# Performance work log

Measured on AMD Instinct MI355X. Metric: run time of the kernel, lower is better.

The kernel has to match this reference:

```python
import jax, jax.numpy as jnp
import numpy as np

B, S, F, E, L, H, DMAX = 8, 1024, 768, 512, 4, 8, 4
HD = E // H
SCALE = HD ** -0.5
EPS = 1e-5


def setup_inputs() -> dict:
    key = jax.random.key(0)
    ks = jax.random.split(key, 20)
    std = 0.02
    inp = {
        "x": jax.random.normal(ks[0], (B, S, F), jnp.float32),
        "distances": jax.random.randint(ks[1], (B, S, S), 0, 8, jnp.int32),
        # lazily-created node-embedding Linear(F -> E)
        "Win": jax.random.normal(ks[2], (F, E), jnp.float32) * std,
        "b_in": jnp.zeros((E,), jnp.float32),
        # per-layer SGT params, stacked on leading layer dim L
        "Wq": jax.random.normal(ks[3], (L, E, E), jnp.float32) * std,
        "bq": jnp.zeros((L, E), jnp.float32),
        "Wk": jax.random.normal(ks[4], (L, E, E), jnp.float32) * std,
        "bk": jnp.zeros((L, E), jnp.float32),
        "Wv": jax.random.normal(ks[5], (L, E, E), jnp.float32) * std,
        "bv": jnp.zeros((L, E), jnp.float32),
        "Wo": jax.random.normal(ks[6], (L, E, E), jnp.float32) * std,
        "bo": jnp.zeros((L, E), jnp.float32),
        "dbias": jax.random.normal(ks[7], (L, DMAX + 1), jnp.float32) * 0.1,
        "ln_g": jnp.ones((L, E), jnp.float32),
        "ln_b": jnp.zeros((L, E), jnp.float32),
        # classifier: Linear(E, E//2) -> ReLU -> Linear(E//2, 2)
        "W1": jax.random.normal(ks[8], (E, E // 2), jnp.float32) * std,
        "b1": jnp.zeros((E // 2,), jnp.float32),
        "W2": jax.random.normal(ks[9], (E // 2, 2), jnp.float32) * std,
        "b2": jnp.zeros((2,), jnp.float32),
    }
    return inp


def _layer_norm(x, g, b):
    m = jnp.mean(x, axis=-1, keepdims=True)
    v = jnp.mean(jnp.square(x - m), axis=-1, keepdims=True)
    return (x - m) * jax.lax.rsqrt(v + EPS) * g + b


def reference(x, distances, Win, b_in, Wq, bq, Wk, bk, Wv, bv, Wo, bo,
              dbias, ln_g, ln_b, W1, b1, W2, b2):
    # input embedding: [B,S,F] -> [B,S,E]
    h = x @ Win + b_in
    d = jnp.clip(distances, 0, DMAX)  # [B,S,S] ints in [0, DMAX]
    for l in range(L):
        # QKV projections, split into heads: [B,H,S,HD]
        q = (h @ Wq[l] + bq[l]).reshape(B, S, H, HD).transpose(0, 2, 1, 3)
        k = (h @ Wk[l] + bk[l]).reshape(B, S, H, HD).transpose(0, 2, 1, 3)
        v = (h @ Wv[l] + bv[l]).reshape(B, S, H, HD).transpose(0, 2, 1, 3)
        # scores + learned distance bias (broadcast over heads)
        scores = jnp.einsum('bhsd,bhtd->bhst', q, k) * SCALE
        scores = scores + dbias[l][d][:, None, :, :]
        attn = jax.nn.softmax(scores, axis=-1)  # dropout = identity (eval)
        o = jnp.einsum('bhst,bhtd->bhsd', attn, v)
        o = o.transpose(0, 2, 1, 3).reshape(B, S, E) @ Wo[l] + bo[l]
        h = _layer_norm(h + o, ln_g[l], ln_b[l])
    # target node is at position 0 of each subgraph
    t = h[:, 0]  # [B,E]
    hid = jax.nn.relu(t @ W1 + b1)
    logits = hid @ W2 + b2  # [B,2]
    return logits
```

## Files before the change

### kernel.cpp

```cpp
#include <hip/hip_runtime.h>
#include <hip/hip_bf16.h>
#include <stdint.h>

#define B_   8
#define S_   1024
#define F_   768
#define E_   512
#define L_   4
#define H_   8
#define HD_  64
#define M_   (B_*S_)
#define SCALE_ 0.125f
#define EPS_ 1e-5f

typedef short bf8_t  __attribute__((ext_vector_type(8)));
typedef float f32x4  __attribute__((ext_vector_type(4)));

static __device__ __forceinline__ uint16_t bfbits(float f) {
    __hip_bfloat16 h = __float2bfloat16(f);
    union { __hip_bfloat16 h; uint16_t u; } cv{h};
    return cv.u;
}
static __device__ __forceinline__ uint32_t pack2bf(float lo, float hi) {
    return (uint32_t)bfbits(lo) | ((uint32_t)bfbits(hi) << 16);
}

template<int ROWS>
static __device__ __forceinline__ void stage_swz(const uint16_t* __restrict__ g, int ldK,
                                                 int k0, char* lds, int tid) {
    const int wave = tid >> 6, lane = tid & 63;
    constexpr int NI = ROWS / 8;
    constexpr int PW = NI / 4;
#pragma unroll
    for (int j = 0; j < PW; ++j) {
        const int I = wave * PW + j;
        const int m = I * 8 + (lane >> 3);
        const int slot = lane & 7;
        const int kc8 = slot ^ (m & 7);
        const uint16_t* gp = g + (size_t)m * ldK + k0 + kc8 * 8;
        __builtin_amdgcn_global_load_lds((const __attribute__((address_space(1))) void*)gp,
                                         (__attribute__((address_space(3))) void*)(lds + I * 1024),
                                         16, 0, 0);
    }
}

template<int OUT_MODE>
__global__ __launch_bounds__(256, 2)
void gemm_mfma(const uint16_t* __restrict__ A, const uint16_t* __restrict__ Wt,
               const float* __restrict__ bias, void* __restrict__ Cout,
               void* __restrict__ Cout2, int K)
{
    __shared__ __align__(16) char smA[128 * 128];
    __shared__ __align__(16) char smB[64 * 128];

    const int tid = threadIdx.x;
    const int lane = tid & 63;
    const int g = lane >> 4;
    const int l15 = lane & 15;
    const int wave = tid >> 6;
    const int wm = wave >> 1;
    const int wn = wave & 1;
    const int n0 = blockIdx.x * 64;
    const int m0 = blockIdx.y * 128;

    f32x4 acc[4][2];
#pragma unroll
    for (int i = 0; i < 4; ++i) {
        acc[i][0] = f32x4{0.f, 0.f, 0.f, 0.f};
        acc[i][1] = f32x4{0.f, 0.f, 0.f, 0.f};
    }

    for (int k0 = 0; k0 < K; k0 += 64) {
        stage_swz<128>(A  + (size_t)m0 * K, K, k0, smA, tid);
        stage_swz< 64>(Wt + (size_t)n0 * K, K, k0, smB, tid);
        __syncthreads();

#pragma unroll
        for (int c = 0; c < 2; ++c) {
            bf8_t bfr[2];
#pragma unroll
            for (int nb = 0; nb < 2; ++nb) {
                const int n = wn * 32 + nb * 16 + l15;
                const int slot = (c * 4 + g) ^ (n & 7);
                bfr[nb] = *(const bf8_t*)(smB + n * 128 + slot * 16);
            }
#pragma unroll
            for (int mi = 0; mi < 4; ++mi) {
                const int m = wm * 64 + mi * 16 + l15;
                const int slot = (c * 4 + g) ^ (m & 7);
                bf8_t af = *(const bf8_t*)(smA + m * 128 + slot * 16);
#pragma unroll
                for (int nb = 0; nb < 2; ++nb)
                    acc[mi][nb] = __builtin_amdgcn_mfma_f32_16x16x32_bf16(af, bfr[nb], acc[mi][nb], 0, 0, 0);
            }
        }
        __syncthreads();
    }

    const int colbase = n0 + wn * 32;
    float bia[2] = { bias[colbase + l15], bias[colbase + 16 + l15] };

#pragma unroll
    for (int mi = 0; mi < 4; ++mi) {
#pragma unroll
        for (int nb = 0; nb < 2; ++nb) {
            const int col  = colbase + nb * 16 + l15;
            const int row0 = m0 + wm * 64 + mi * 16 + g * 4;
            f32x4 v = acc[mi][nb];
            const float r0 = v.x + bia[nb], r1 = v.y + bia[nb];
            const float r2 = v.z + bia[nb], r3 = v.w + bia[nb];
            if (OUT_MODE == 1) {
                float* C = (float*)Cout;
                C[(size_t)(row0+0)*E_ + col] = r0;
                C[(size_t)(row0+1)*E_ + col] = r1;
                C[(size_t)(row0+2)*E_ + col] = r2;
                C[(size_t)(row0+3)*E_ + col] = r3;
            } else {
                float* C = (float*)Cout;
                uint16_t* C2 = (uint16_t*)Cout2;
                C[(size_t)(row0+0)*E_ + col] = r0;
                C[(size_t)(row0+1)*E_ + col] = r1;
                C[(size_t)(row0+2)*E_ + col] = r2;
                C[(size_t)(row0+3)*E_ + col] = r3;
                C2[(size_t)(row0+0)*E_ + col] = bfbits(r0);
                C2[(size_t)(row0+1)*E_ + col] = bfbits(r1);
                C2[(size_t)(row0+2)*E_ + col] = bfbits(r2);
                C2[(size_t)(row0+3)*E_ + col] = bfbits(r3);
            }
        }
    }
}

__global__ __launch_bounds__(256, 2)
void gemm_qkv(const uint16_t* __restrict__ A, const uint16_t* __restrict__ Wt,
              const float* __restrict__ bqp, const float* __restrict__ bkp,
              const float* __restrict__ bvp,
              uint16_t* __restrict__ qb, uint16_t* __restrict__ kb,
              uint16_t* __restrict__ vTb)
{
    __shared__ __align__(16) char smA[128 * 128];
    __shared__ __align__(16) char smB[64 * 128];

    const int tid = threadIdx.x;
    const int lane = tid & 63;
    const int g = lane >> 4;
    const int l15 = lane & 15;
    const int wave = tid >> 6;
    const int wm = wave >> 1;
    const int wn = wave & 1;
    const int n0 = blockIdx.x * 64;
    const int m0 = blockIdx.y * 128;
    const int sec = n0 >> 9;

    f32x4 acc[4][2];
#pragma unroll
    for (int i = 0; i < 4; ++i) {
        acc[i][0] = f32x4{0.f, 0.f, 0.f, 0.f};
        acc[i][1] = f32x4{0.f, 0.f, 0.f, 0.f};
    }

    for (int k0 = 0; k0 < E_; k0 += 64) {
        stage_swz<128>(A  + (size_t)m0 * E_, E_, k0, smA, tid);
        stage_swz< 64>(Wt + (size_t)n0 * E_, E_, k0, smB, tid);
        __syncthreads();

#pragma unroll
        for (int c = 0; c < 2; ++c) {
            bf8_t bfr[2];
#pragma unroll
            for (int nb = 0; nb < 2; ++nb) {
                const int n = wn * 32 + nb * 16 + l15;
                const int slot = (c * 4 + g) ^ (n & 7);
                bfr[nb] = *(const bf8_t*)(smB + n * 128 + slot * 16);
            }
#pragma unroll
            for (int mi = 0; mi < 4; ++mi) {
                const int m = wm * 64 + mi * 16 + l15;
                const int slot = (c * 4 + g) ^ (m & 7);
                bf8_t af = *(const bf8_t*)(smA + m * 128 + slot * 16);
#pragma unroll
                for (int nb = 0; nb < 2; ++nb)
                    acc[mi][nb] = __builtin_amdgcn_mfma_f32_16x16x32_bf16(af, bfr[nb], acc[mi][nb], 0, 0, 0);
            }
        }
        __syncthreads();
    }

    const float* bp = sec == 0 ? bqp : sec == 1 ? bkp : bvp;
    const int colbase = n0 + wn * 32;
    const int cb511 = colbase & 511;
    float bia[2] = { bp[cb511 + l15], bp[cb511 + 16 + l15] };

#pragma unroll
    for (int mi = 0; mi < 4; ++mi) {
#pragma unroll
        for (int nb = 0; nb < 2; ++nb) {
            const int col  = cb511 + nb * 16 + l15;
            const int row0 = m0 + wm * 64 + mi * 16 + g * 4;
            f32x4 v = acc[mi][nb];
            const float r0 = v.x + bia[nb], r1 = v.y + bia[nb];
            const float r2 = v.z + bia[nb], r3 = v.w + bia[nb];
            if (sec < 2) {
                uint16_t* C = sec == 0 ? qb : kb;
                C[(size_t)(row0+0)*E_ + col] = bfbits(r0);
                C[(size_t)(row0+1)*E_ + col] = bfbits(r1);
                C[(size_t)(row0+2)*E_ + col] = bfbits(r2);
                C[(size_t)(row0+3)*E_ + col] = bfbits(r3);
            } else {
                const int b  = row0 >> 10;
                const int s0 = row0 & 1023;
                uint2 val{pack2bf(r0, r1), pack2bf(r2, r3)};
                *(uint2*)&vTb[((size_t)(b * E_ + col)) * S_ + s0] = val;
            }
        }
    }
}

__global__ __launch_bounds__(256, 3)
void attn_mfma(const uint16_t* __restrict__ q, const uint16_t* __restrict__ k,
               const uint16_t* __restrict__ vT, const uint8_t* __restrict__ dT,
               const float* __restrict__ dbias, int layer, uint16_t* __restrict__ ob)
{
    __shared__ __align__(16) char Kb[2][64 * 128];
    __shared__ __align__(16) char Vb[2][64 * 128];

    const int tid = threadIdx.x, lane = tid & 63;
    const int g = lane >> 4, l15 = lane & 15, wq = tid >> 6;
    const int bid = blockIdx.x;
    const int qt = bid & 15, hh = (bid >> 4) & 7, b = bid >> 7;
    const int qrow = qt * 64 + wq * 16 + l15;

    const float db0 = dbias[layer*5+0], db1 = dbias[layer*5+1], db2 = dbias[layer*5+2],
                db3 = dbias[layer*5+3], db4 = dbias[layer*5+4];

    bf8_t qf[2];
    const uint16_t* qbase = q + ((size_t)(b * S_ + qrow)) * E_ + hh * 64;
#pragma unroll
    for (int c = 0; c < 2; ++c) qf[c] = *(const bf8_t*)(qbase + c * 32 + g * 8);

    f32x4 accO[4];
#pragma unroll
    for (int f = 0; f < 4; ++f) accO[f] = f32x4{0.f, 0.f, 0.f, 0.f};
    float mrun = -1e30f, lrun = 0.f;

    const uint16_t* kTile = k  + ((size_t)(b * S_)) * E_ + hh * 64;
    const uint16_t* vTile = vT + ((size_t)(b * E_ + hh * 64)) * S_;
    const uint8_t*  dbase = dT + ((size_t)(b * S_)) * S_ + qt * 64 + wq * 16 + l15;

    stage_swz<64>(kTile, E_, 0, Kb[0], tid);
    stage_swz<64>(vTile, S_, 0, Vb[0], tid);
    int dcur[16];
#pragma unroll
    for (int f = 0; f < 4; ++f)
#pragma unroll
        for (int r = 0; r < 4; ++r)
            dcur[f*4+r] = dbase[(size_t)(f*16 + g*4 + r) * S_];
    __syncthreads();

    for (int t = 0; t < 16; ++t) {
        const int cur = t & 1;
        char* kc_ = Kb[cur];
        char* vc_ = Vb[cur];
        if (t < 15) {
            stage_swz<64>(kTile + (size_t)(t + 1) * 64 * E_, E_, 0, Kb[cur ^ 1], tid);
            stage_swz<64>(vTile, S_, (t + 1) * 64, Vb[cur ^ 1], tid);
        }
        int dnxt[16];
#pragma unroll
        for (int f = 0; f < 4; ++f)
#pragma unroll
            for (int r = 0; r < 4; ++r)
                dnxt[f*4+r] = (t < 15) ? (int)dbase[(size_t)((t+1)*64 + f*16 + g*4 + r) * S_] : 0;

        f32x4 sc[4];
#pragma unroll
        for (int f = 0; f < 4; ++f) sc[f] = f32x4{0.f, 0.f, 0.f, 0.f};
        __builtin_amdgcn_s_setprio(1);
#pragma unroll
        for (int f = 0; f < 4; ++f) {
#pragma unroll
            for (int c = 0; c < 2; ++c) {
                const int slot = (c * 4 + g) ^ (l15 & 7);
                bf8_t kf = *(const bf8_t*)(kc_ + (f*16 + l15) * 128 + slot * 16);
                sc[f] = __builtin_amdgcn_mfma_f32_16x16x32_bf16(kf, qf[c], sc[f], 0, 0, 0);
            }
        }
        __builtin_amdgcn_s_setprio(0);

        float p[4][4];
        float tmax = -1e30f;
#pragma unroll
        for (int f = 0; f < 4; ++f) {
#pragma unroll
            for (int r = 0; r < 4; ++r) {
                const int d = dcur[f*4+r];
                const float bsel = d==0 ? db0 : d==1 ? db1 : d==2 ? db2 : d==3 ? db3 : db4;
                const float sv = fmaf(sc[f][r], SCALE_, bsel);
                p[f][r] = sv;
                tmax = fmaxf(tmax, sv);
            }
        }
        tmax = fmaxf(tmax, __shfl_xor(tmax, 16, 64));
        tmax = fmaxf(tmax, __shfl_xor(tmax, 32, 64));
        const float mnew = fmaxf(mrun, tmax);
        const float corr = __expf(mrun - mnew);
        float psum = 0.f;
#pragma unroll
        for (int f = 0; f < 4; ++f)
#pragma unroll
            for (int r = 0; r < 4; ++r) {
                p[f][r] = __expf(p[f][r] - mnew);
                psum += p[f][r];
            }
        psum += __shfl_xor(psum, 16, 64);
        psum += __shfl_xor(psum, 32, 64);
        lrun = fmaf(lrun, corr, psum);
        mrun = mnew;
#pragma unroll
        for (int f = 0; f < 4; ++f) accO[f] *= corr;

        uint32_t pk[4][2];
#pragma unroll
        for (int f = 0; f < 4; ++f) {
            pk[f][0] = pack2bf(p[f][0], p[f][1]);
            pk[f][1] = pack2bf(p[f][2], p[f][3]);
        }
        bf8_t pB[2];
#pragma unroll
        for (int c = 0; c < 2; ++c) {
            union { uint32_t w[4]; bf8_t v; } u;
#pragma unroll
            for (int j = 0; j < 4; ++j) {
                const int src = (((2*g + (j >> 1)) & 3) * 16) + l15;
                const uint32_t a  = (uint32_t)__shfl((int)pk[c*2+0][j & 1], src, 64);
                const uint32_t bb = (uint32_t)__shfl((int)pk[c*2+1][j & 1], src, 64);
                u.w[j] = (g >= 2) ? bb : a;
            }
            pB[c] = u.v;
        }

        __builtin_amdgcn_s_setprio(1);
#pragma unroll
        for (int c = 0; c < 2; ++c) {
#pragma unroll
            for (int f = 0; f < 4; ++f) {
                const int slot = (c * 4 + g) ^ (l15 & 7);
                bf8_t vf = *(const bf8_t*)(vc_ + (f*16 + l15) * 128 + slot * 16);
                accO[f] = __builtin_amdgcn_mfma_f32_16x16x32_bf16(vf, pB[c], accO[f], 0, 0, 0);
            }
        }
        __builtin_amdgcn_s_setprio(0);

        __syncthreads();
#pragma unroll
        for (int i = 0; i < 16; ++i) dcur[i] = dnxt[i];
    }

    const float inv = 1.f / lrun;
    uint16_t* obase = ob + ((size_t)(b * S_ + qrow)) * E_ + hh * 64;
#pragma unroll
    for (int f = 0; f < 4; ++f) {
        f32x4 v = accO[f];
        uint2 val{pack2bf(v.x * inv, v.y * inv), pack2bf(v.z * inv, v.w * inv)};
        *(uint2*)(obase + f * 16 + g * 4) = val;
    }
}

__global__ __launch_bounds__(256, 4)
void dist_transpose(const int* __restrict__ dist, uint8_t* __restrict__ dT)
{
    __shared__ uint8_t sT[64][64];
    const int tid = threadIdx.x;
    const int q0 = blockIdx.x * 64, t0 = blockIdx.y * 64, b = blockIdx.z;
    const int r = tid >> 4, c4 = tid & 15;
#pragma unroll
    for (int i = 0; i < 4; ++i) {
        const int qq = r + i * 16;
        int4 d4 = *(const int4*)&dist[((size_t)(b * S_ + q0 + qq)) * S_ + t0 + c4 * 4];
        sT[c4*4+0][qq] = (uint8_t)min(max(d4.x, 0), 4);
        sT[c4*4+1][qq] = (uint8_t)min(max(d4.y, 0), 4);
        sT[c4*4+2][qq] = (uint8_t)min(max(d4.z, 0), 4);
        sT[c4*4+3][qq] = (uint8_t)min(max(d4.w, 0), 4);
    }
    __syncthreads();
    const int kk = tid >> 2, qc = tid & 3;
    int4 v = *(const int4*)&sT[kk][qc * 16];
    *(int4*)&dT[((size_t)(b * S_ + t0 + kk)) * S_ + q0 + qc * 16] = v;
}

__global__ void convert_bf16(const float* __restrict__ src, uint16_t* __restrict__ dst, int n8)
{
    const int i = blockIdx.x * 256 + threadIdx.x;
    if (i >= n8) return;
    float4 a = *(const float4*)&src[(size_t)i * 8];
    float4 b = *(const float4*)&src[(size_t)i * 8 + 4];
    uint4 o{pack2bf(a.x, a.y), pack2bf(a.z, a.w), pack2bf(b.x, b.y), pack2bf(b.z, b.w)};
    *(uint4*)&dst[(size_t)i * 8] = o;
}

__global__ __launch_bounds__(256, 2)
void wtrans(const float* __restrict__ Win, const float* __restrict__ Wq,
            const float* __restrict__ Wk, const float* __restrict__ Wv,
            const float* __restrict__ Wo, uint16_t* __restrict__ Wt)
{
    __shared__ float ls[64][65];
    const int idx = blockIdx.z;
    const int Ki = (idx == 0) ? F_ : E_;
    if (blockIdx.x * 64 >= Ki) return;
    const float* src;
    size_t dstoff;
    if (idx == 0) { src = Win; dstoff = 0; }
    else {
        const int l = (idx - 1) >> 2, which = (idx - 1) & 3;
        if (which == 0)      { src = Wq + (size_t)l*E_*E_; dstoff = (size_t)F_*E_ + (size_t)(l*3+0)*E_*E_; }
        else if (which == 1) { src = Wk + (size_t)l*E_*E_; dstoff = (size_t)F_*E_ + (size_t)(l*3+1)*E_*E_; }
        else if (which == 2) { src = Wv + (size_t)l*E_*E_; dstoff = (size_t)F_*E_ + (size_t)(l*3+2)*E_*E_; }
        else                 { src = Wo + (size_t)l*E_*E_; dstoff = (size_t)F_*E_ + (size_t)12*E_*E_ + (size_t)l*E_*E_; }
    }
    uint16_t* dst = Wt + dstoff;
    const int k0 = blockIdx.x * 64, n0 = blockIdx.y * 64;
    const int tid = threadIdx.x;
    const int r = tid >> 4, c4 = tid & 15;
#pragma unroll
    for (int i = 0; i < 4; ++i)
        *(float4*)&ls[r + i*16][c4*4] = *(const float4*)&src[(size_t)(k0 + r + i*16) * E_ + n0 + c4*4];
    __syncthreads();
#pragma unroll
    for (int i = 0; i < 2; ++i) {
        const int chunk = tid + 256 * i;
        const int n = chunk >> 3, kc = chunk & 7;
        uint4 o{pack2bf(ls[kc*8+0][n], ls[kc*8+1][n]),
                pack2bf(ls[kc*8+2][n], ls[kc*8+3][n]),
                pack2bf(ls[kc*8+4][n], ls[kc*8+5][n]),
                pack2bf(ls[kc*8+6][n], ls[kc*8+7][n])};
        *(uint4*)&dst[((size_t)(n0 + n)) * Ki + k0 + kc * 8] = o;
    }
}

__global__ __launch_bounds__(256, 8)
void residual_ln(float* __restrict__ h, const float* __restrict__ o,
                 const float* __restrict__ g, const float* __restrict__ beta,
                 uint16_t* __restrict__ hb)
{
    const int wave = threadIdx.x >> 6;
    const int lane = threadIdx.x & 63;
    const int row  = blockIdx.x * 4 + wave;

    float* hr = h + (size_t)row * E_;
    const float* orow = o + (size_t)row * E_;

    float x[8];
    {
        float4 a  = *(const float4*)&hr[lane*4];
        float4 b4 = *(const float4*)&hr[256 + lane*4];
        float4 oa = *(const float4*)&orow[lane*4];
        float4 obv = *(const float4*)&orow[256 + lane*4];
        x[0] = a.x + oa.x; x[1] = a.y + oa.y; x[2] = a.z + oa.z; x[3] = a.w + oa.w;
        x[4] = b4.x + obv.x; x[5] = b4.y + obv.y; x[6] = b4.z + obv.z; x[7] = b4.w + obv.w;
    }
    float sum = 0.f, sq = 0.f;
#pragma unroll
    for (int i = 0; i < 8; ++i) { sum += x[i]; sq += x[i]*x[i]; }
#pragma unroll
    for (int off = 1; off < 64; off <<= 1) {
        sum += __shfl_xor(sum, off, 64);
        sq  += __shfl_xor(sq,  off, 64);
    }
    const float mean = sum * (1.f/512.f);
    const float var  = sq * (1.f/512.f) - mean*mean;
    const float inv  = rsqrtf(var + EPS_);

    float4 g0 = *(const float4*)&g[lane*4];
    float4 g1 = *(const float4*)&g[256 + lane*4];
    float4 be0 = *(const float4*)&beta[lane*4];
    float4 be1 = *(const float4*)&beta[256 + lane*4];

    float4 y0, y1;
    y0.x = (x[0]-mean)*inv*g0.x + be0.x;
    y0.y = (x[1]-mean)*inv*g0.y + be0.y;
    y0.z = (x[2]-mean)*inv*g0.z + be0.z;
    y0.w = (x[3]-mean)*inv*g0.w + be0.w;
    y1.x = (x[4]-mean)*inv*g1.x + be1.x;
    y1.y = (x[5]-mean)*inv*g1.y + be1.y;
    y1.z = (x[6]-mean)*inv*g1.z + be1.z;
    y1.w = (x[7]-mean)*inv*g1.w + be1.w;
    *(float4*)&hr[lane*4] = y0;
    *(float4*)&hr[256 + lane*4] = y1;

    uint16_t* hrow = hb + (size_t)row * E_;
    uint2 p0{pack2bf(y0.x, y0.y), pack2bf(y0.z, y0.w)};
    uint2 p1{pack2bf(y1.x, y1.y), pack2bf(y1.z, y1.w)};
    *(uint2*)&hrow[lane*4]       = p0;
    *(uint2*)&hrow[256 + lane*4] = p1;
}

__global__ __launch_bounds__(256, 1)
void head_kernel(const float* __restrict__ h, const float* __restrict__ W1,
                 const float* __restrict__ b1, const float* __restrict__ W2,
                 const float* __restrict__ b2, float* __restrict__ out)
{
    __shared__ float tl[512];
    __shared__ float red[8];
    const int tid = threadIdx.x;
    const int b = blockIdx.x;

    const float* hr = h + (size_t)b * S_ * E_;
    *(float2*)&tl[tid*2] = *(const float2*)&hr[tid*2];
    __syncthreads();

    float acc = b1[tid];
    for (int kk = 0; kk < 512; ++kk)
        acc = fmaf(tl[kk], W1[kk * 256 + tid], acc);
    float hid = fmaxf(acc, 0.f);

    float p0 = hid * W2[tid*2 + 0];
    float p1 = hid * W2[tid*2 + 1];
#pragma unroll
    for (int off = 32; off; off >>= 1) {
        p0 += __shfl_down(p0, off, 64);
        p1 += __shfl_down(p1, off, 64);
    }
    if ((tid & 63) == 0) {
        red[(tid >> 6)*2 + 0] = p0;
        red[(tid >> 6)*2 + 1] = p1;
    }
    __syncthreads();
    if (tid == 0) {
        out[b*2 + 0] = red[0] + red[2] + red[4] + red[6] + b2[0];
        out[b*2 + 1] = red[1] + red[3] + red[5] + red[7] + b2[1];
    }
}

extern "C" void kernel_launch(void* const* d_in, const int* in_sizes, int n_in,
                              void* d_out, int out_size, void* d_ws, size_t ws_size,
                              hipStream_t stream)
{
    const float* x     = (const float*)d_in[0];
    const int*   dist  = (const int*)  d_in[1];
    const float* Win   = (const float*)d_in[2];
    const float* b_in  = (const float*)d_in[3];
    const float* Wq    = (const float*)d_in[4];
    const float* bq    = (const float*)d_in[5];
    const float* Wk    = (const float*)d_in[6];
    const float* bk    = (const float*)d_in[7];
    const float* Wv    = (const float*)d_in[8];
    const float* bv    = (const float*)d_in[9];
    const float* Wo    = (const float*)d_in[10];
    const float* bo    = (const float*)d_in[11];
    const float* dbias = (const float*)d_in[12];
    const float* ln_g  = (const float*)d_in[13];
    const float* ln_b  = (const float*)d_in[14];
    const float* W1    = (const float*)d_in[15];
    const float* b1    = (const float*)d_in[16];
    const float* W2    = (const float*)d_in[17];
    const float* b2    = (const float*)d_in[18];
    float* out = (float*)d_out;

    char* w8 = (char*)d_ws;
    float*    h    = (float*)   (w8);
    float*    pb   = (float*)   (w8 + (size_t)(16<<20));
    uint16_t* hbf  = (uint16_t*)(w8 + (size_t)(32<<20));
    uint16_t* qb   = (uint16_t*)(w8 + (size_t)(40<<20));
    uint16_t* kb   = (uint16_t*)(w8 + (size_t)(48<<20));
    uint16_t* vTb  = (uint16_t*)(w8 + (size_t)(56<<20));
    uint16_t* obuf = (uint16_t*)(w8 + (size_t)(64<<20));
    uint16_t* xb   = (uint16_t*)(w8 + (size_t)(72<<20));
    uint16_t* Wt   = (uint16_t*)(w8 + (size_t)(84<<20));
    uint8_t*  dT   = (uint8_t*) (w8 + (size_t)(93<<20));

    const dim3 blk(256);
    const dim3 ggrid(E_/64, M_/128);
    const dim3 qkvgrid(3*E_/64, M_/128);

    convert_bf16<<<dim3(M_*F_/8/256), blk, 0, stream>>>(x, xb, M_*F_/8);
    wtrans<<<dim3(12, 8, 17), blk, 0, stream>>>(Win, Wq, Wk, Wv, Wo, Wt);
    dist_transpose<<<dim3(16, 16, 8), blk, 0, stream>>>(dist, dT);

    gemm_mfma<2><<<ggrid, blk, 0, stream>>>(xb, Wt, b_in, h, hbf, F_);

    for (int l = 0; l < L_; ++l) {
        const uint16_t* Wqkv = Wt + (size_t)F_*E_ + (size_t)(l*3)*E_*E_;
        const uint16_t* Wto  = Wt + (size_t)F_*E_ + (size_t)12*E_*E_ + (size_t)l*E_*E_;
        gemm_qkv<<<qkvgrid, blk, 0, stream>>>(hbf, Wqkv, bq + l*E_, bk + l*E_, bv + l*E_,
                                              qb, kb, vTb);
        attn_mfma<<<dim3(B_*H_*16), blk, 0, stream>>>(qb, kb, vTb, dT, dbias, l, obuf);
        gemm_mfma<1><<<ggrid, blk, 0, stream>>>(obuf, Wto, bo + l*E_, pb, nullptr, E_);
        residual_ln<<<dim3(M_/4), blk, 0, stream>>>(h, pb, ln_g + l*E_, ln_b + l*E_, hbf);
    }

    head_kernel<<<dim3(B_), blk, 0, stream>>>(h, W1, b1, W2, b2, out);
}
```

Before: 615.7 us.

## Precompute bf16 distance bias, fold scale into Q, lazy softmax rescale, wider QKV tiles

Replaces the transposed uint8 distance map with a per-layer bf16 bias tensor, already scaled by log2e, that attention adds directly into the score accumulators. The softmax scale times log2e is folded into Q in the QKV GEMM epilogue, so attention can use exp2 and drops its per-element bias selection and multiply. The running-max rescale is skipped unless the new max exceeds the old one by a threshold. Separately, the QKV GEMM tile widens to 128 columns, the attention block order is remapped, and attention occupancy is raised. The trade-off is extra memory traffic each layer, since the int32 distances are reread and a 16 MB bias is written and then read, plus bf16 rounding of the bias values.

```diff
diff --git a/kernel.cpp b/kernel.cpp
--- a/kernel.cpp
+++ b/kernel.cpp
@@ -10,8 +10,9 @@
 #define H_   8
 #define HD_  64
 #define M_   (B_*S_)
-#define SCALE_ 0.125f
 #define EPS_ 1e-5f
+#define LOG2E_ 1.44269504089f
+#define SL2E_  (0.125f * LOG2E_)
 
 typedef short bf8_t  __attribute__((ext_vector_type(8)));
 typedef float f32x4  __attribute__((ext_vector_type(4)));
@@ -23,6 +24,10 @@
 }
 static __device__ __forceinline__ uint32_t pack2bf(float lo, float hi) {
     return (uint32_t)bfbits(lo) | ((uint32_t)bfbits(hi) << 16);
+}
+static __device__ __forceinline__ float asf(uint32_t u) {
+    union { uint32_t u; float f; } cv{u};
+    return cv.f;
 }
 
 template<int ROWS>
@@ -139,7 +144,7 @@
               uint16_t* __restrict__ vTb)
 {
     __shared__ __align__(16) char smA[128 * 128];
-    __shared__ __align__(16) char smB[64 * 128];
+    __shared__ __align__(16) char smB[128 * 128];
 
     const int tid = threadIdx.x;
     const int lane = tid & 63;
@@ -148,30 +153,28 @@
     const int wave = tid >> 6;
     const int wm = wave >> 1;
     const int wn = wave & 1;
-    const int n0 = blockIdx.x * 64;
+    const int n0 = blockIdx.x * 128;
     const int m0 = blockIdx.y * 128;
-    const int sec = n0 >> 9;
-
-    f32x4 acc[4][2];
-#pragma unroll
-    for (int i = 0; i < 4; ++i) {
-        acc[i][0] = f32x4{0.f, 0.f, 0.f, 0.f};
-        acc[i][1] = f32x4{0.f, 0.f, 0.f, 0.f};
-    }
+
+    f32x4 acc[4][4];
+#pragma unroll
+    for (int i = 0; i < 4; ++i)
+#pragma unroll
+        for (int j = 0; j < 4; ++j) acc[i][j] = f32x4{0.f, 0.f, 0.f, 0.f};
 
     for (int k0 = 0; k0 < E_; k0 += 64) {
         stage_swz<128>(A  + (size_t)m0 * E_, E_, k0, smA, tid);
-        stage_swz< 64>(Wt + (size_t)n0 * E_, E_, k0, smB, tid);
+        stage_swz<128>(Wt + (size_t)n0 * E_, E_, k0, smB, tid);
         __syncthreads();
 
 #pragma unroll
         for (int c = 0; c < 2; ++c) {
-            bf8_t bfr[2];
-#pragma unroll
-            for (int nb = 0; nb < 2; ++nb) {
-                const int n = wn * 32 + nb * 16 + l15;
+            bf8_t bfr[4];
+#pragma unroll
+            for (int nj = 0; nj < 4; ++nj) {
+                const int n = wn * 64 + nj * 16 + l15;
                 const int slot = (c * 4 + g) ^ (n & 7);
-                bfr[nb] = *(const bf8_t*)(smB + n * 128 + slot * 16);
+                bfr[nj] = *(const bf8_t*)(smB + n * 128 + slot * 16);
             }
 #pragma unroll
             for (int mi = 0; mi < 4; ++mi) {
@@ -179,27 +182,27 @@
                 const int slot = (c * 4 + g) ^ (m & 7);
                 bf8_t af = *(const bf8_t*)(smA + m * 128 + slot * 16);
 #pragma unroll
-                for (int nb = 0; nb < 2; ++nb)
-                    acc[mi][nb] = __builtin_amdgcn_mfma_f32_16x16x32_bf16(af, bfr[nb], acc[mi][nb], 0, 0, 0);
+                for (int nj = 0; nj < 4; ++nj)
+                    acc[mi][nj] = __builtin_amdgcn_mfma_f32_16x16x32_bf16(af, bfr[nj], acc[mi][nj], 0, 0, 0);
             }
         }
         __syncthreads();
     }
 
+    const int sec = (n0 + wn * 64) >> 9;
     const float* bp = sec == 0 ? bqp : sec == 1 ? bkp : bvp;
-    const int colbase = n0 + wn * 32;
-    const int cb511 = colbase & 511;
-    float bia[2] = { bp[cb511 + l15], bp[cb511 + 16 + l15] };
+    const int cbase = (n0 + wn * 64) & 511;
 
 #pragma unroll
     for (int mi = 0; mi < 4; ++mi) {
 #pragma unroll
-        for (int nb = 0; nb < 2; ++nb) {
-            const int col  = cb511 + nb * 16 + l15;
+        for (int nj = 0; nj < 4; ++nj) {
+            const int col  = cbase + nj * 16 + l15;
             const int row0 = m0 + wm * 64 + mi * 16 + g * 4;
-            f32x4 v = acc[mi][nb];
-            const float r0 = v.x + bia[nb], r1 = v.y + bia[nb];
-            const float r2 = v.z + bia[nb], r3 = v.w + bia[nb];
+            const float bia = bp[col];
+            f32x4 v = acc[mi][nj];
+            float r0 = v.x + bia, r1 = v.y + bia, r2 = v.z + bia, r3 = v.w + bia;
+            if (sec == 0) { r0 *= SL2E_; r1 *= SL2E_; r2 *= SL2E_; r3 *= SL2E_; }
             if (sec < 2) {
                 uint16_t* C = sec == 0 ? qb : kb;
                 C[(size_t)(row0+0)*E_ + col] = bfbits(r0);
@@ -216,23 +219,47 @@
     }
 }
 
-__global__ __launch_bounds__(256, 3)
+__global__ __launch_bounds__(256, 8)
+void dist_bias_layer(const int* __restrict__ dist, const float* __restrict__ dbias5,
+                     uint16_t* __restrict__ biasL)
+{
+    const size_t base = ((size_t)blockIdx.x * 256 + threadIdx.x) * 16;
+    const float t0 = dbias5[0] * LOG2E_, t1 = dbias5[1] * LOG2E_,
+                t2 = dbias5[2] * LOG2E_, t3 = dbias5[3] * LOG2E_,
+                t4 = dbias5[4] * LOG2E_;
+    uint32_t w[8];
+#pragma unroll
+    for (int j = 0; j < 4; ++j) {
+        int4 v = *(const int4*)&dist[base + j * 4];
+        const int d0 = min(max(v.x, 0), 4), d1 = min(max(v.y, 0), 4);
+        const int d2 = min(max(v.z, 0), 4), d3 = min(max(v.w, 0), 4);
+        const float s0 = d0==0 ? t0 : d0==1 ? t1 : d0==2 ? t2 : d0==3 ? t3 : t4;
+        const float s1 = d1==0 ? t0 : d1==1 ? t1 : d1==2 ? t2 : d1==3 ? t3 : t4;
+        const float s2 = d2==0 ? t0 : d2==1 ? t1 : d2==2 ? t2 : d2==3 ? t3 : t4;
+        const float s3 = d3==0 ? t0 : d3==1 ? t1 : d3==2 ? t2 : d3==3 ? t3 : t4;
+        w[j*2+0] = pack2bf(s0, s1);
+        w[j*2+1] = pack2bf(s2, s3);
+    }
+    uint16_t* dst = biasL + base;
+    *(uint4*)dst       = uint4{w[0], w[1], w[2], w[3]};
+    *(uint4*)(dst + 8) = uint4{w[4], w[5], w[6], w[7]};
+}
+
+__global__ __launch_bounds__(256, 4)
 void attn_mfma(const uint16_t* __restrict__ q, const uint16_t* __restrict__ k,
-               const uint16_t* __restrict__ vT, const uint8_t* __restrict__ dT,
-               const float* __restrict__ dbias, int layer, uint16_t* __restrict__ ob)
+               const uint16_t* __restrict__ vT, const uint16_t* __restrict__ biasL,
+               uint16_t* __restrict__ ob)
 {
     __shared__ __align__(16) char Kb[2][64 * 128];
     __shared__ __align__(16) char Vb[2][64 * 128];
 
     const int tid = threadIdx.x, lane = tid & 63;
     const int g = lane >> 4, l15 = lane & 15, wq = tid >> 6;
-    const int bid = blockIdx.x;
+    const int bid0 = blockIdx.x;
+    const int bid = (bid0 & 7) * 256 + (bid0 >> 3);
     const int qt = bid & 15, hh = (bid >> 4) & 7, b = bid >> 7;
     const int qrow = qt * 64 + wq * 16 + l15;
 
-    const float db0 = dbias[layer*5+0], db1 = dbias[layer*5+1], db2 = dbias[layer*5+2],
-                db3 = dbias[layer*5+3], db4 = dbias[layer*5+4];
-
     bf8_t qf[2];
     const uint16_t* qbase = q + ((size_t)(b * S_ + qrow)) * E_ + hh * 64;
 #pragma unroll
@@ -245,16 +272,14 @@
 
     const uint16_t* kTile = k  + ((size_t)(b * S_)) * E_ + hh * 64;
     const uint16_t* vTile = vT + ((size_t)(b * E_ + hh * 64)) * S_;
-    const uint8_t*  dbase = dT + ((size_t)(b * S_)) * S_ + qt * 64 + wq * 16 + l15;
+    const uint16_t* bbase = biasL + ((size_t)b << 20) + ((size_t)qrow << 10);
 
     stage_swz<64>(kTile, E_, 0, Kb[0], tid);
     stage_swz<64>(vTile, S_, 0, Vb[0], tid);
-    int dcur[16];
+    uint2 bcur[4];
 #pragma unroll
     for (int f = 0; f < 4; ++f)
-#pragma unroll
-        for (int r = 0; r < 4; ++r)
-            dcur[f*4+r] = dbase[(size_t)(f*16 + g*4 + r) * S_];
+        bcur[f] = *(const uint2*)(bbase + f * 16 + g * 4);
     __syncthreads();
 
     for (int t = 0; t < 16; ++t) {
@@ -265,16 +290,19 @@
             stage_swz<64>(kTile + (size_t)(t + 1) * 64 * E_, E_, 0, Kb[cur ^ 1], tid);
             stage_swz<64>(vTile, S_, (t + 1) * 64, Vb[cur ^ 1], tid);
         }
-        int dnxt[16];
+        uint2 bnxt[4];
 #pragma unroll
         for (int f = 0; f < 4; ++f)
-#pragma unroll
-            for (int r = 0; r < 4; ++r)
-                dnxt[f*4+r] = (t < 15) ? (int)dbase[(size_t)((t+1)*64 + f*16 + g*4 + r) * S_] : 0;
+            bnxt[f] = (t < 15) ? *(const uint2*)(bbase + (t + 1) * 64 + f * 16 + g * 4)
+                               : uint2{0, 0};
 
         f32x4 sc[4];
 #pragma unroll
-        for (int f = 0; f < 4; ++f) sc[f] = f32x4{0.f, 0.f, 0.f, 0.f};
+        for (int f = 0; f < 4; ++f) {
+            const uint2 w = bcur[f];
+            sc[f] = f32x4{asf(w.x << 16), asf(w.x & 0xffff0000u),
+                          asf(w.y << 16), asf(w.y & 0xffff0000u)};
+        }
         __builtin_amdgcn_s_setprio(1);
 #pragma unroll
         for (int f = 0; f < 4; ++f) {
@@ -287,37 +315,33 @@
         }
         __builtin_amdgcn_s_setprio(0);
 
-        float p[4][4];
         float tmax = -1e30f;
 #pragma unroll
         for (int f = 0; f < 4; ++f) {
-#pragma unroll
-            for (int r = 0; r < 4; ++r) {
-                const int d = dcur[f*4+r];
-                const float bsel = d==0 ? db0 : d==1 ? db1 : d==2 ? db2 : d==3 ? db3 : db4;
-                const float sv = fmaf(sc[f][r], SCALE_, bsel);
-                p[f][r] = sv;
-                tmax = fmaxf(tmax, sv);
-            }
+            tmax = fmaxf(tmax, fmaxf(fmaxf(sc[f][0], sc[f][1]), fmaxf(sc[f][2], sc[f][3])));
         }
         tmax = fmaxf(tmax, __shfl_xor(tmax, 16, 64));
         tmax = fmaxf(tmax, __shfl_xor(tmax, 32, 64));
-        const float mnew = fmaxf(mrun, tmax);
-        const float corr = __expf(mrun - mnew);
+        if (__any(tmax > mrun + 11.0f)) {
+            const float mnew = fmaxf(mrun, tmax);
+            const float corr = exp2f(mrun - mnew);
+            lrun *= corr;
+#pragma unroll
+            for (int f = 0; f < 4; ++f) accO[f] *= corr;
+            mrun = mnew;
+        }
+        float p[4][4];
         float psum = 0.f;
 #pragma unroll
         for (int f = 0; f < 4; ++f)
 #pragma unroll
             for (int r = 0; r < 4; ++r) {
-                p[f][r] = __expf(p[f][r] - mnew);
+                p[f][r] = exp2f(sc[f][r] - mrun);
                 psum += p[f][r];
             }
         psum += __shfl_xor(psum, 16, 64);
         psum += __shfl_xor(psum, 32, 64);
-        lrun = fmaf(lrun, corr, psum);
-        mrun = mnew;
-#pragma unroll
-        for (int f = 0; f < 4; ++f) accO[f] *= corr;
+        lrun += psum;
 
         uint32_t pk[4][2];
 #pragma unroll
@@ -353,7 +377,7 @@
 
         __syncthreads();
 #pragma unroll
-        for (int i = 0; i < 16; ++i) dcur[i] = dnxt[i];
+        for (int f = 0; f < 4; ++f) bcur[f] = bnxt[f];
     }
 
     const float inv = 1.f / lrun;
@@ -364,28 +388,6 @@
         uint2 val{pack2bf(v.x * inv, v.y * inv), pack2bf(v.z * inv, v.w * inv)};
         *(uint2*)(obase + f * 16 + g * 4) = val;
     }
-}
-
-__global__ __launch_bounds__(256, 4)
-void dist_transpose(const int* __restrict__ dist, uint8_t* __restrict__ dT)
-{
-    __shared__ uint8_t sT[64][64];
-    const int tid = threadIdx.x;
-    const int q0 = blockIdx.x * 64, t0 = blockIdx.y * 64, b = blockIdx.z;
-    const int r = tid >> 4, c4 = tid & 15;
-#pragma unroll
-    for (int i = 0; i < 4; ++i) {
-        const int qq = r + i * 16;
-        int4 d4 = *(const int4*)&dist[((size_t)(b * S_ + q0 + qq)) * S_ + t0 + c4 * 4];
-        sT[c4*4+0][qq] = (uint8_t)min(max(d4.x, 0), 4);
-        sT[c4*4+1][qq] = (uint8_t)min(max(d4.y, 0), 4);
-        sT[c4*4+2][qq] = (uint8_t)min(max(d4.z, 0), 4);
-        sT[c4*4+3][qq] = (uint8_t)min(max(d4.w, 0), 4);
-    }
-    __syncthreads();
-    const int kk = tid >> 2, qc = tid & 3;
-    int4 v = *(const int4*)&sT[kk][qc * 16];
-    *(int4*)&dT[((size_t)(b * S_ + t0 + kk)) * S_ + q0 + qc * 16] = v;
 }
 
 __global__ void convert_bf16(const float* __restrict__ src, uint16_t* __restrict__ dst, int n8)
@@ -557,33 +559,33 @@
     float* out = (float*)d_out;
 
     char* w8 = (char*)d_ws;
-    float*    h    = (float*)   (w8);
-    float*    pb   = (float*)   (w8 + (size_t)(16<<20));
-    uint16_t* hbf  = (uint16_t*)(w8 + (size_t)(32<<20));
-    uint16_t* qb   = (uint16_t*)(w8 + (size_t)(40<<20));
-    uint16_t* kb   = (uint16_t*)(w8 + (size_t)(48<<20));
-    uint16_t* vTb  = (uint16_t*)(w8 + (size_t)(56<<20));
-    uint16_t* obuf = (uint16_t*)(w8 + (size_t)(64<<20));
-    uint16_t* xb   = (uint16_t*)(w8 + (size_t)(72<<20));
-    uint16_t* Wt   = (uint16_t*)(w8 + (size_t)(84<<20));
-    uint8_t*  dT   = (uint8_t*) (w8 + (size_t)(93<<20));
+    float*    h     = (float*)   (w8);
+    float*    pb    = (float*)   (w8 + (size_t)(16<<20));
+    uint16_t* xb    = (uint16_t*)(w8 + (size_t)(16<<20));
+    uint16_t* hbf   = (uint16_t*)(w8 + (size_t)(32<<20));
+    uint16_t* qb    = (uint16_t*)(w8 + (size_t)(40<<20));
+    uint16_t* kb    = (uint16_t*)(w8 + (size_t)(48<<20));
+    uint16_t* vTb   = (uint16_t*)(w8 + (size_t)(56<<20));
+    uint16_t* obuf  = (uint16_t*)(w8 + (size_t)(64<<20));
+    uint16_t* Wt    = (uint16_t*)(w8 + (size_t)(72<<20));
+    uint16_t* biasL = (uint16_t*)(w8 + (size_t)(82<<20));
 
     const dim3 blk(256);
     const dim3 ggrid(E_/64, M_/128);
-    const dim3 qkvgrid(3*E_/64, M_/128);
+    const dim3 qkvgrid(3*E_/128, M_/128);
 
     convert_bf16<<<dim3(M_*F_/8/256), blk, 0, stream>>>(x, xb, M_*F_/8);
     wtrans<<<dim3(12, 8, 17), blk, 0, stream>>>(Win, Wq, Wk, Wv, Wo, Wt);
-    dist_transpose<<<dim3(16, 16, 8), blk, 0, stream>>>(dist, dT);
 
     gemm_mfma<2><<<ggrid, blk, 0, stream>>>(xb, Wt, b_in, h, hbf, F_);
 
     for (int l = 0; l < L_; ++l) {
         const uint16_t* Wqkv = Wt + (size_t)F_*E_ + (size_t)(l*3)*E_*E_;
         const uint16_t* Wto  = Wt + (size_t)F_*E_ + (size_t)12*E_*E_ + (size_t)l*E_*E_;
+        dist_bias_layer<<<dim3((B_*S_*S_/16)/256), blk, 0, stream>>>(dist, dbias + l*5, biasL);
         gemm_qkv<<<qkvgrid, blk, 0, stream>>>(hbf, Wqkv, bq + l*E_, bk + l*E_, bv + l*E_,
                                               qb, kb, vTb);
-        attn_mfma<<<dim3(B_*H_*16), blk, 0, stream>>>(qb, kb, vTb, dT, dbias, l, obuf);
+        attn_mfma<<<dim3(B_*H_*16), blk, 0, stream>>>(qb, kb, vTb, biasL, obuf);
         gemm_mfma<1><<<ggrid, blk, 0, stream>>>(obuf, Wto, bo + l*E_, pb, nullptr, E_);
         residual_ln<<<dim3(M_/4), blk, 0, stream>>>(h, pb, ln_g + l*E_, ln_b + l*E_, hbf);
     }
```

Result: no change. 609.7 us (-1.0%).
